# Optimization experiments

Measured on AMD Instinct MI355X. Metric: run time of the kernel, lower is better.

Reference implementation:

```python
import jax, jax.numpy as jnp
import numpy as np

# ---- config (matches init_kwargs) ----
GROUP_NUM = 2048
K_NEIGHBORS = 32
OUT_DIM = 192
SIGMA, BASELINE, SCALING, EPS = 0.26, 0.1, 10.0, 1e-6
ALPHA, BETA = 1000.0, 100.0
ADAPTIVE_RATIO = 0.5
IN_DIM = 3
ADAPTIVE_DIM = int(OUT_DIM * ADAPTIVE_RATIO)          # 96
FOURIER_DIM = OUT_DIM - ADAPTIVE_DIM                  # 96
FEAT_DIM_F = FOURIER_DIM // (IN_DIM * 2)              # 16
FEAT_DIM_A = int(np.ceil(ADAPTIVE_DIM / IN_DIM))      # 32
FEAT_NUM_A = FEAT_DIM_A * IN_DIM                      # 96
OUT_IDX = np.linspace(0, FEAT_NUM_A - 1, ADAPTIVE_DIM).astype(np.int64)


def setup_inputs() -> dict:
    key = jax.random.key(0)
    k1, k2, k3, k4 = jax.random.split(key, 4)
    xyz = jax.random.normal(k1, (4, 8192, 3), dtype=jnp.float32)
    x = jax.random.normal(k2, (4, 8192, 96), dtype=jnp.float32)
    bn_gamma = jax.random.uniform(k3, (192,), dtype=jnp.float32)
    bn_beta = jax.random.normal(k4, (192,), dtype=jnp.float32)
    return {"xyz": xyz, "x": x, "bn_gamma": bn_gamma, "bn_beta": bn_beta}


def _fps(xyz, m):
    """Farthest point sampling. xyz: [B,N,3] -> idx [B,m] (int32). Seed = index 0."""
    def single(pts):
        n = pts.shape[0]
        def step(carry, _):
            dists, last = carry
            d = jnp.sum((pts - pts[last]) ** 2, axis=-1)
            dists = jnp.minimum(dists, d)
            nxt = jnp.argmax(dists).astype(jnp.int32)
            return (dists, nxt), nxt
        init = (jnp.full((n,), 1e10, pts.dtype), jnp.array(0, jnp.int32))
        _, idxs = jax.lax.scan(step, init, None, length=m - 1)
        return jnp.concatenate([jnp.zeros((1,), jnp.int32), idxs])
    return jax.vmap(single)(xyz)


def _square_distance(src, dst):
    # src: [B,S,3], dst: [B,N,3] -> [B,S,N]
    d = -2.0 * jnp.einsum('bsc,bnc->bsn', src, dst)
    d += jnp.sum(src ** 2, -1)[:, :, None]
    d += jnp.sum(dst ** 2, -1)[:, None, :]
    return d


def _gather_knn(points, idx):
    # points: [B,N,C], idx: [B,G,K] -> [B,G,K,C]
    return jax.vmap(lambda p, i: p[i])(points, idx)


def _forward(xyz, x, bn_gamma, bn_beta):
    B, N, _ = xyz.shape
    G, K = GROUP_NUM, K_NEIGHBORS

    # ---- Grouper_seg ----
    fps_idx = _fps(xyz, G)                                   # [B,G]
    lc_xyz = jnp.take_along_axis(xyz, fps_idx[..., None], 1)  # [B,G,3]
    lc_x = jnp.take_along_axis(x, fps_idx[..., None], 1)      # [B,G,C]
    sqr = _square_distance(lc_xyz, xyz)                       # [B,G,N]
    knn_idx = jax.lax.top_k(-sqr, K)[1]                       # [B,G,K] smallest-k
    knn_xyz = _gather_knn(xyz, knn_idx)                       # [B,G,K,3]
    knn_x = _gather_knn(x, knn_idx)                           # [B,G,K,C]

    # ---- Aggregation_seg: local normalization ----
    mean_x = lc_x[:, :, None, :]
    std_x = jnp.std(knn_x - mean_x, ddof=1)
    mean_xyz = lc_xyz[:, :, None, :]
    std_xyz = jnp.std(knn_xyz - mean_xyz, ddof=1)
    knn_x = (knn_x - mean_x) / (std_x + 1e-5)
    knn_xyz_n = (knn_xyz - mean_xyz) / (std_xyz + 1e-5)       # [B,G,K,3]
    C = knn_x.shape[-1]
    knn_x = jnp.concatenate(
        [knn_x, jnp.broadcast_to(lc_x[:, :, None, :], (B, G, K, C))], axis=-1)  # [B,G,K,2C]
    knn_xyz_cf = jnp.transpose(knn_xyz_n, (0, 3, 1, 2))       # [B,3,G,K]
    knn_x_cf = jnp.transpose(knn_x, (0, 3, 1, 2))             # [B,OUT_DIM,G,K]

    # ---- PosE_Geo: fourier part ----
    feat_range = jnp.arange(FEAT_DIM_F, dtype=knn_xyz_cf.dtype)
    dim_embed = ALPHA ** (feat_range / FEAT_DIM_F)            # [F]
    div = BETA * knn_xyz_cf[..., None] / dim_embed            # [B,3,G,K,F]
    fourier = jnp.stack([jnp.sin(div), jnp.cos(div)], axis=-1)  # [B,3,G,K,F,2]
    fourier = fourier.reshape(B, IN_DIM, G, K, 2 * FEAT_DIM_F)
    fourier = jnp.transpose(fourier, (0, 1, 4, 2, 3)).reshape(B, FOURIER_DIM, G, K)

    # ---- AdaptiveEmbedding (parameterless, data-driven) ----
    x4 = knn_xyz_n                                            # [B,G,K,3]
    gstd = jnp.mean(jnp.std(x4.reshape(B, -1, IN_DIM), axis=1, ddof=1))
    sig = SIGMA * (1.0 + gstd) + EPS
    blend = jax.nn.sigmoid((gstd - BASELINE) * SCALING)
    feat_val = jnp.linspace(-1.0, 1.0, FEAT_DIM_A + 2)[1:-1]  # [Fa]
    z = (x4[..., None] - feat_val) / sig                      # [B,G,K,3,Fa]
    comb = blend * jnp.exp(-0.5 * z * z) + (1.0 - blend) * jnp.cos(z)
    ae = comb.reshape(B, G, K, FEAT_NUM_A)[..., OUT_IDX]      # [B,G,K,ADAPTIVE_DIM]
    ae_cf = jnp.transpose(ae, (0, 3, 1, 2))                   # [B,ADAPTIVE_DIM,G,K]

    pe = jnp.concatenate([fourier, ae_cf], axis=1)            # [B,OUT_DIM,G,K]
    knn_x_w = (knn_x_cf + pe) * pe

    # ---- Pooling_seg: max+mean pool, BatchNorm1d (train stats) + GELU ----
    lc = jnp.max(knn_x_w, -1) + jnp.mean(knn_x_w, -1)         # [B,OUT_DIM,G]
    mu = jnp.mean(lc, axis=(0, 2), keepdims=True)
    var = jnp.var(lc, axis=(0, 2), keepdims=True)
    y = (lc - mu) / jnp.sqrt(var + 1e-5)
    y = y * bn_gamma[None, :, None] + bn_beta[None, :, None]
    return jax.nn.gelu(y, approximate=False)


def reference(xyz, x, bn_gamma, bn_beta):
    return _forward(xyz, x, bn_gamma, bn_beta)
```

## Files before the change

### kernel.cpp

```cpp
#include <hip/hip_runtime.h>
#include <cstdint>
#include <math.h>

#define NPTS 8192
#define NB 4
#define NG 2048
#define NK 32
#define CIN 96
#define COUT 192

typedef unsigned long long ull;

__global__ __launch_bounds__(256) void setup_kernel(const float* __restrict__ xyz,
                                                    float* __restrict__ xs, float* __restrict__ ys,
                                                    float* __restrict__ zs, float* __restrict__ d2){
  int i = blockIdx.x*256 + threadIdx.x;
  if (i >= NB*NPTS) return;
  float x = xyz[3*i+0], y = xyz[3*i+1], z = xyz[3*i+2];
  xs[i]=x; ys[i]=y; zs[i]=z;
  d2[i] = __fadd_rn(__fadd_rn(__fmul_rn(x,x),__fmul_rn(y,y)),__fmul_rn(z,z));
}

template<int CTRL>
__device__ __forceinline__ ull dppmax64(ull v){
  unsigned lo=(unsigned)v, hi=(unsigned)(v>>32);
  unsigned olo=(unsigned)__builtin_amdgcn_update_dpp((int)lo,(int)lo,CTRL,0xf,0xf,false);
  unsigned ohi=(unsigned)__builtin_amdgcn_update_dpp((int)hi,(int)hi,CTRL,0xf,0xf,false);
  ull o=((ull)ohi<<32)|(ull)olo;
  return (o>v)?o:v;
}
__device__ __forceinline__ ull wavemax64(ull v){
  v=dppmax64<0x111>(v); v=dppmax64<0x112>(v); v=dppmax64<0x114>(v);
  v=dppmax64<0x118>(v); v=dppmax64<0x142>(v); v=dppmax64<0x143>(v);
  return v;
}

__global__ __launch_bounds__(512,2) void fps_kernel(const float* __restrict__ xyz, int* __restrict__ fps_idx){
#pragma clang fp contract(off)
  extern __shared__ char smem[];
  float4* ctab = (float4*)smem;
  ull*    keys = (ull*)(smem + 131072);
  int*    hist = (int*)(smem + 131072 + 128);
  float*  bbs  = (float*)(smem + 131072 + 128 + 2048);
  float*  bbc  = (float*)(smem + 131072 + 128 + 2048 + 192);
  const int b = blockIdx.x, t = threadIdx.x;
  const int w = t>>6, lane = t&63;
  const float* base = xyz + (size_t)b*NPTS*3;

  float ox[16], oy[16], oz[16];
#pragma unroll
  for (int j=0;j<16;++j){
    int p = t + 512*j;
    ox[j]=base[3*p+0]; oy[j]=base[3*p+1]; oz[j]=base[3*p+2];
  }
  float mnx=ox[0],mxx=ox[0],mny=oy[0],mxy=oy[0],mnz=oz[0],mxz=oz[0];
#pragma unroll
  for (int j=1;j<16;++j){
    mnx=fminf(mnx,ox[j]); mxx=fmaxf(mxx,ox[j]);
    mny=fminf(mny,oy[j]); mxy=fmaxf(mxy,oy[j]);
    mnz=fminf(mnz,oz[j]); mxz=fmaxf(mxz,oz[j]);
  }
#pragma unroll
  for (int off=32; off>0; off>>=1){
    mnx=fminf(mnx,__shfl_xor(mnx,off)); mxx=fmaxf(mxx,__shfl_xor(mxx,off));
    mny=fminf(mny,__shfl_xor(mny,off)); mxy=fmaxf(mxy,__shfl_xor(mxy,off));
    mnz=fminf(mnz,__shfl_xor(mnz,off)); mxz=fmaxf(mxz,__shfl_xor(mxz,off));
  }
  hist[t] = 0;
  if (lane==0){
    bbs[w*6+0]=mnx; bbs[w*6+1]=mxx; bbs[w*6+2]=mny;
    bbs[w*6+3]=mxy; bbs[w*6+4]=mnz; bbs[w*6+5]=mxz;
  }
  if (t==0) fps_idx[b*NG] = 0;
  __syncthreads();
  float gx0=1e30f,gx1=-1e30f,gy0=1e30f,gy1=-1e30f,gz0=1e30f,gz1=-1e30f;
  for (int q=0;q<8;++q){
    gx0=fminf(gx0,bbs[q*6+0]); gx1=fmaxf(gx1,bbs[q*6+1]);
    gy0=fminf(gy0,bbs[q*6+2]); gy1=fmaxf(gy1,bbs[q*6+3]);
    gz0=fminf(gz0,bbs[q*6+4]); gz1=fmaxf(gz1,bbs[q*6+5]);
  }
  const float sxv = 8.0f/fmaxf(gx1-gx0,1e-20f);
  const float syv = 8.0f/fmaxf(gy1-gy0,1e-20f);
  const float szv = 8.0f/fmaxf(gz1-gz0,1e-20f);
  int cell[16];
#pragma unroll
  for (int j=0;j<16;++j){
    int cx = min(7,(int)((ox[j]-gx0)*sxv));
    int cy = min(7,(int)((oy[j]-gy0)*syv));
    int cz = min(7,(int)((oz[j]-gz0)*szv));
    int m = (cx&1) | ((cy&1)<<1) | ((cz&1)<<2)
          | ((cx&2)<<2) | ((cy&2)<<3) | ((cz&2)<<4)
          | ((cx&4)<<4) | ((cy&4)<<5) | ((cz&4)<<6);
    cell[j]=m;
    atomicAdd(&hist[m],1);
  }
  __syncthreads();
  if (t==0){
    int run=0;
    for (int c=0;c<512;++c){ int h=hist[c]; hist[c]=run; run+=h; }
  }
  __syncthreads();
#pragma unroll
  for (int j=0;j<16;++j){
    int pos = atomicAdd(&hist[cell[j]],1);
    ctab[pos] = make_float4(ox[j],oy[j],oz[j], __int_as_float(t+512*j));
  }
  __syncthreads();
  float px[16],py[16],pz[16],D[16]; unsigned lowb[16];
#pragma unroll
  for (int j=0;j<16;++j){
    int pos = (w<<10) + (j<<6) + lane;
    float4 c4 = ctab[pos];
    px[j]=c4.x; py[j]=c4.y; pz[j]=c4.z;
    unsigned orig = (unsigned)__float_as_int(c4.w);
    lowb[j] = ((8191u-orig)<<13) | (unsigned)pos;
    D[j] = 1e10f;
  }
#pragma unroll
  for (int j=0;j<16;++j){
    float a0=px[j],a1=px[j],b0=py[j],b1=py[j],c0=pz[j],c1=pz[j];
#pragma unroll
    for (int off=32; off>0; off>>=1){
      a0=fminf(a0,__shfl_xor(a0,off)); a1=fmaxf(a1,__shfl_xor(a1,off));
      b0=fminf(b0,__shfl_xor(b0,off)); b1=fmaxf(b1,__shfl_xor(b1,off));
      c0=fminf(c0,__shfl_xor(c0,off)); c1=fmaxf(c1,__shfl_xor(c1,off));
    }
    if (lane==0){
      float* o = bbc + (w*16+j)*6;
      o[0]=a0; o[1]=a1; o[2]=b0; o[3]=b1; o[4]=c0; o[5]=c1;
    }
  }
  __syncthreads();
  float cb0=0,cb1=0,cb2=0,cb3=0,cb4=0,cb5=0;
  if (lane<16){
    const float* o = bbc + (w*16+lane)*6;
    cb0=o[0]; cb1=o[1]; cb2=o[2]; cb3=o[3]; cb4=o[4]; cb5=o[5];
  }

  float lx=base[0], ly=base[1], lz=base[2];
  ull ckey = (((ull)__float_as_uint(1e10f))<<32);
  for (int it=0; it<NG-1; ++it){
    float Mthr = __int_as_float((unsigned)(ckey>>32)) * 1.0001f;
    float qx=fminf(fmaxf(lx,cb0),cb1);
    float qy=fminf(fmaxf(ly,cb2),cb3);
    float qz=fminf(fmaxf(lz,cb4),cb5);
    float ddx=qx-lx, ddy=qy-ly, ddz=qz-lz;
    float LB=(ddx*ddx+ddy*ddy)+ddz*ddz;
    ull bal = __ballot(LB <= Mthr);
    unsigned mask = __builtin_amdgcn_readfirstlane((unsigned)bal) & 0xFFFFu;
    ull* kslot = &keys[(it&1)*8 + w];
    if (mask){
#pragma unroll
      for (int j=0;j<16;++j){
        if (mask & (1u<<j)){
          float dx=px[j]-lx, dy=py[j]-ly, dz=pz[j]-lz;
          float d=(dx*dx+dy*dy)+dz*dz;
          D[j]=fminf(D[j],d);
        }
      }
      ull P = (((ull)__float_as_uint(D[0]))<<32) | (ull)lowb[0];
#pragma unroll
      for (int j=1;j<16;++j){
        ull c = (((ull)__float_as_uint(D[j]))<<32) | (ull)lowb[j];
        if (c > P) P = c;
      }
      P = wavemax64(P);
      if (lane==63) *kslot = P;
      unsigned khi = (unsigned)__builtin_amdgcn_readlane((int)(P>>32),63);
      unsigned klo = (unsigned)__builtin_amdgcn_readlane((int)P,63);
      ckey = (((ull)khi)<<32)|(ull)klo;
    } else {
      if (lane==63) *kslot = ckey;
    }
    __syncthreads();
    const ull* kk = keys + (it&1)*8;
    ull k = kk[0];
#pragma unroll
    for (int q=1;q<8;++q){ ull o=kk[q]; if (o>k) k=o; }
    unsigned lw = (unsigned)k;
    float4 c4 = ctab[lw & 0x1FFFu];
    lx=c4.x; ly=c4.y; lz=c4.z;
    if (t==0) fps_idx[b*NG + it + 1] = (int)(8191u - ((lw>>13)&0x1FFFu));
  }
}

__device__ __forceinline__ bool lexlt(float ad, int ai, float bd, int bi){
  return (ad < bd) || ((ad == bd) && (ai < bi));
}
__device__ __forceinline__ void sort_desc(float& d, int& i, int lane){
#pragma unroll
  for (int k=2;k<=64;k<<=1){
#pragma unroll
    for (int j=k>>1;j>0;j>>=1){
      float od = __shfl_xor(d, j);
      int   oi = __shfl_xor(i, j);
      bool dirUp = (lane & k) != 0;
      bool lower = (lane & j) == 0;
      bool less  = lexlt(d,i,od,oi);
      bool keep  = (less == (lower == dirUp));
      if (!keep){ d=od; i=oi; }
    }
  }
}
__device__ __forceinline__ void merge_asc(float& d, int& i, int lane){
#pragma unroll
  for (int j=32;j>0;j>>=1){
    float od = __shfl_xor(d, j);
    int   oi = __shfl_xor(i, j);
    bool lower = (lane & j) == 0;
    bool less  = lexlt(d,i,od,oi);
    bool keep  = (less == lower);
    if (!keep){ d=od; i=oi; }
  }
}

__global__ __launch_bounds__(256) void knn_kernel(const float* __restrict__ xs, const float* __restrict__ ys,
                                                  const float* __restrict__ zs, const float* __restrict__ d2,
                                                  const int* __restrict__ fps_idx, int* __restrict__ knn_out){
  __shared__ float tx[256], ty[256], tz[256], td[256];
  const int tid = threadIdx.x;
  const int wid = tid>>6, lane = tid&63;
  const int pid = blockIdx.x*4 + wid;
  const int b = pid >> 11;
  const float* bx = xs + b*NPTS;
  const float* by = ys + b*NPTS;
  const float* bz = zs + b*NPTS;
  const float* bD = d2 + b*NPTS;
  const int fi = fps_idx[pid];
  const float ax = bx[fi], ay = by[fi], az = bz[fi];
  const float src2 = __fadd_rn(__fadd_rn(__fmul_rn(ax,ax),__fmul_rn(ay,ay)),__fmul_rn(az,az));
  float Ad = INFINITY; int Ai = 0x7fffffff;
  float tau_d = INFINITY; int tau_i = 0x7fffffff;
  for (int s=0; s<NPTS/256; ++s){
    __syncthreads();
    int gidx = s*256 + tid;
    tx[tid]=bx[gidx]; ty[tid]=by[gidx]; tz[tid]=bz[gidx]; td[tid]=bD[gidx];
    __syncthreads();
    float m0,m1,m2,m3; int i0,i1,i2,i3;
#define LOADJ(mj, ij, J) { int li = (J)*64 + lane; \
    float dot = __fadd_rn(__fadd_rn(__fmul_rn(ax,tx[li]),__fmul_rn(ay,ty[li])),__fmul_rn(az,tz[li])); \
    mj = __fadd_rn(__fadd_rn(__fmul_rn(-2.0f,dot), src2), td[li]); ij = s*256 + li; }
    LOADJ(m0,i0,0) LOADJ(m1,i1,1) LOADJ(m2,i2,2) LOADJ(m3,i3,3)
#undef LOADJ
    while (true){
      bool any = lexlt(m0,i0,tau_d,tau_i) || lexlt(m1,i1,tau_d,tau_i) ||
                 lexlt(m2,i2,tau_d,tau_i) || lexlt(m3,i3,tau_d,tau_i);
      if (__ballot(any) == 0ull) break;
      float cd = m0; int ci = i0; int sel = 0;
      if (lexlt(m1,i1,cd,ci)){ cd=m1; ci=i1; sel=1; }
      if (lexlt(m2,i2,cd,ci)){ cd=m2; ci=i2; sel=2; }
      if (lexlt(m3,i3,cd,ci)){ cd=m3; ci=i3; sel=3; }
      if      (sel==0) m0=INFINITY;
      else if (sel==1) m1=INFINITY;
      else if (sel==2) m2=INFINITY;
      else             m3=INFINITY;
      sort_desc(cd, ci, lane);
      if (lexlt(cd,ci,Ad,Ai)){ Ad=cd; Ai=ci; }
      merge_asc(Ad, Ai, lane);
      tau_d = __shfl(Ad, 31);
      tau_i = __shfl(Ai, 31);
    }
  }
  if (lane < NK) knn_out[pid*NK + lane] = Ai;
}

__global__ __launch_bounds__(256) void stats_kernel(const float* __restrict__ x, const float* __restrict__ xyz,
                                                    const int* __restrict__ fps_idx, const int* __restrict__ knn,
                                                    double* __restrict__ partials){
  const int tid=threadIdx.x, wid=tid>>6, lane=tid&63;
  const int pid = blockIdx.x*4 + wid;
  const int b = pid>>11;
  const int fi = fps_idx[pid];
  const float* xb = x + (size_t)b*NPTS*CIN;
  const float* zb = xyz + (size_t)b*NPTS*3;
  const float lc0 = xb[fi*CIN + lane];
  float lc1 = 0.f; if (lane<32) lc1 = xb[fi*CIN + 64 + lane];
  float czv = 0.f; if (lane<3)  czv = zb[fi*3 + lane];
  double s1=0.0, s2=0.0, a1=0.0, a2=0.0;
  for (int k=0;k<NK;++k){
    int idx = knn[pid*NK + k];
    float d0 = __fsub_rn(xb[idx*CIN + lane], lc0);
    s1 += (double)d0; s2 += (double)d0*(double)d0;
    if (lane<32){
      float d1 = __fsub_rn(xb[idx*CIN + 64 + lane], lc1);
      s1 += (double)d1; s2 += (double)d1*(double)d1;
    }
    if (lane<3){
      float w = __fsub_rn(zb[idx*3 + lane], czv);
      a1 += (double)w; a2 += (double)w*(double)w;
    }
  }
#pragma unroll
  for (int off=32; off>0; off>>=1){ s1 += __shfl_xor(s1,off); s2 += __shfl_xor(s2,off); }
  __shared__ double shx[4][2];
  __shared__ double shz[4][3][2];
  if (lane==0){ shx[wid][0]=s1; shx[wid][1]=s2; }
  if (lane<3){ shz[wid][lane][0]=a1; shz[wid][lane][1]=a2; }
  __syncthreads();
  if (tid==0){
    double u0=0,u1=0;
    for (int w=0;w<4;++w){ u0+=shx[w][0]; u1+=shx[w][1]; }
    double* outp = partials + (size_t)blockIdx.x*8;
    outp[0]=u0; outp[1]=u1;
    for (int axq=0; axq<3; ++axq){
      double v0=0,v1=0;
      for (int w=0;w<4;++w){ v0+=shz[w][axq][0]; v1+=shz[w][axq][1]; }
      outp[2+2*axq]=v0; outp[3+2*axq]=v1;
    }
  }
}

__global__ void finalize_kernel(const double* __restrict__ partials, float* __restrict__ scal){
  const int lane = threadIdx.x;
  double s1=0,s2=0;
  double z0a=0,z0b=0,z1a=0,z1b=0,z2a=0,z2b=0;
  for (int i=0;i<32;++i){
    const double* p = partials + (size_t)(lane*32+i)*8;
    s1+=p[0]; s2+=p[1];
    z0a+=p[2]; z0b+=p[3]; z1a+=p[4]; z1b+=p[5]; z2a+=p[6]; z2b+=p[7];
  }
#pragma unroll
  for (int off=32; off>0; off>>=1){ s1+=__shfl_xor(s1,off); s2+=__shfl_xor(s2,off); }
#pragma unroll
  for (int off=8; off>0; off>>=1){
    z0a+=__shfl_xor(z0a,off); z0b+=__shfl_xor(z0b,off);
    z1a+=__shfl_xor(z1a,off); z1b+=__shfl_xor(z1b,off);
    z2a+=__shfl_xor(z2a,off); z2b+=__shfl_xor(z2b,off);
  }
  __shared__ double zb[4][3][2];
  if ((lane&15)==0){
    int b = lane>>4;
    zb[b][0][0]=z0a; zb[b][0][1]=z0b;
    zb[b][1][0]=z1a; zb[b][1][1]=z1b;
    zb[b][2][0]=z2a; zb[b][2][1]=z2b;
  }
  __syncthreads();
  if (lane==0){
    double nx = (double)NB*NG*NK*CIN;
    double varx = (s2 - s1*s1/nx)/(nx-1.0);
    float stdx = (float)sqrt(varx);
    double t1=0,t2=0;
    for (int b=0;b<4;++b) for (int a=0;a<3;++a){ t1+=zb[b][a][0]; t2+=zb[b][a][1]; }
    double nz = (double)NB*NG*NK*3;
    double varz = (t2 - t1*t1/nz)/(nz-1.0);
    float stdz = (float)sqrt(varz);
    float sdiv = stdz + 1e-5f;
    double n2 = (double)NG*NK;
    double acc=0.0;
    for (int b=0;b<4;++b) for (int a=0;a<3;++a){
      double v = (zb[b][a][1] - zb[b][a][0]*zb[b][a][0]/n2)/(n2-1.0);
      acc += sqrt(v);
    }
    float gstd = (float)(acc/12.0) / sdiv;
    float sig = 0.26f*(1.0f+gstd) + 1e-6f;
    float blend = 1.0f/(1.0f + expf(-(gstd-0.1f)*10.0f));
    scal[0] = 1.0f/(stdx + 1e-5f);
    scal[1] = 1.0f/sdiv;
    scal[2] = 1.0f/sig;
    scal[3] = blend;
  }
}

__global__ __launch_bounds__(256) void main_kernel(const float* __restrict__ x, const float* __restrict__ xyz,
                                                   const int* __restrict__ fps_idx, const int* __restrict__ knn,
                                                   const float* __restrict__ scal, float* __restrict__ lc_out){
  const int tid=threadIdx.x, wid=tid>>6, lane=tid&63;
  const int pid = blockIdx.x*4 + wid;
  const int b = pid>>11, g = pid&2047;
  const float inv_x = scal[0], inv_z = scal[1], inv_sig = scal[2], blend = scal[3];
  const float omb = 1.0f - blend;
  const int fi = fps_idx[pid];
  const float* xb = x + (size_t)b*NPTS*CIN;
  const float* zb = xyz + (size_t)b*NPTS*3;
  const float cx = zb[fi*3+0], cy = zb[fi*3+1], cz = zb[fi*3+2];
  const float lcx0 = xb[fi*CIN + lane];
  const float lcx1 = (lane<32) ? xb[fi*CIN + 64 + lane] : xb[fi*CIN + lane - 32];
  const float lcx2 = xb[fi*CIN + 32 + lane];
  const int dim0 = lane>>5;
  const int rr0 = lane&31;
  const bool cos0 = rr0 & 1;
  const float bs0 = 100.0f / powf(1000.0f, (float)(rr0>>1) * (1.0f/16.0f));
  const bool cos1 = lane & 1;
  const float bs1 = 100.0f / powf(1000.0f, (float)((lane&31)>>1) * (1.0f/16.0f));
  const float fv1 = (float)(-1.0 + 2.0*(double)(lane-32+1)/33.0);
  const int dim2 = (32+lane)>>5;
  const int j2 = (32+lane)&31;
  const float fv2 = (float)(-1.0 + 2.0*(double)(j2+1)/33.0);

  float mx0=-INFINITY, mx1=-INFINITY, mx2=-INFINITY;
  float sm0=0.f, sm1=0.f, sm2=0.f;
  for (int k=0;k<NK;++k){
    const int idx = knn[pid*NK + k];
    const float p0 = zb[idx*3+0], p1 = zb[idx*3+1], p2v = zb[idx*3+2];
    const float xn0 = (p0-cx)*inv_z, xn1 = (p1-cy)*inv_z, xn2 = (p2v-cz)*inv_z;
    const float xk0 = xb[idx*CIN + lane];
    float xk1 = 0.f; if (lane<32) xk1 = xb[idx*CIN + 64 + lane];
    {
      float v = dim0 ? xn1 : xn0;
      float a = v * bs0;
      float pe = cos0 ? __cosf(a) : __sinf(a);
      float f = (xk0 - lcx0) * inv_x;
      float w = (f + pe) * pe;
      mx0 = fmaxf(mx0, w); sm0 += w;
    }
    {
      float pe, f;
      if (lane < 32){
        float a = xn2 * bs1;
        pe = cos1 ? __cosf(a) : __sinf(a);
        f = (xk1 - lcx1) * inv_x;
      } else {
        float zq = (xn0 - fv1) * inv_sig;
        pe = blend * __expf(-0.5f*zq*zq) + omb * __cosf(zq);
        f = lcx1;
      }
      float w = (f + pe) * pe;
      mx1 = fmaxf(mx1, w); sm1 += w;
    }
    {
      float v = (dim2==1) ? xn1 : xn2;
      float zq = (v - fv2) * inv_sig;
      float pe = blend * __expf(-0.5f*zq*zq) + omb * __cosf(zq);
      float w = (lcx2 + pe) * pe;
      mx2 = fmaxf(mx2, w); sm2 += w;
    }
  }
  const size_t obase = ((size_t)b*COUT)*NG + g;
  lc_out[obase + (size_t)lane*NG]       = mx0 + sm0*(1.0f/32.0f);
  lc_out[obase + (size_t)(64+lane)*NG]  = mx1 + sm1*(1.0f/32.0f);
  lc_out[obase + (size_t)(128+lane)*NG] = mx2 + sm2*(1.0f/32.0f);
}

__global__ __launch_bounds__(256) void bn_stats_kernel(const float* __restrict__ lc, float* __restrict__ bn){
  const int c = blockIdx.x, t = threadIdx.x, lane=t&63, wid=t>>6;
  double s1=0.0, s2=0.0;
  for (int i=t; i<NB*NG; i+=256){
    int b=i>>11, g=i&2047;
    float v = lc[((size_t)(b*COUT)+c)*NG + g];
    s1 += (double)v; s2 += (double)v*(double)v;
  }
#pragma unroll
  for (int off=32; off>0; off>>=1){ s1+=__shfl_xor(s1,off); s2+=__shfl_xor(s2,off); }
  __shared__ double sh1[4], sh2[4];
  if (lane==0){ sh1[wid]=s1; sh2[wid]=s2; }
  __syncthreads();
  if (t==0){
    double a=sh1[0]+sh1[1]+sh1[2]+sh1[3], q=sh2[0]+sh2[1]+sh2[2]+sh2[3];
    double n=(double)(NB*NG);
    double mu=a/n, var=q/n - mu*mu;
    bn[c]=(float)mu;
    bn[COUT+c]=(float)(1.0/sqrt(var + 1e-5));
  }
}

__global__ __launch_bounds__(256) void final_kernel(const float* __restrict__ bn, const float* __restrict__ gamma,
                                                    const float* __restrict__ beta, float* __restrict__ out){
  int i = blockIdx.x*256 + threadIdx.x;
  int c = (i >> 11) % COUT;
  float v = out[i];
  float y = (v - bn[c]) * bn[COUT + c];
  y = y*gamma[c] + beta[c];
  out[i] = y * 0.5f * (1.0f + erff(y * 0.70710678118654752f));
}

extern "C" void kernel_launch(void* const* d_in, const int* in_sizes, int n_in,
                              void* d_out, int out_size, void* d_ws, size_t ws_size,
                              hipStream_t stream){
  const float* xyz   = (const float*)d_in[0];
  const float* x     = (const float*)d_in[1];
  const float* gamma = (const float*)d_in[2];
  const float* beta  = (const float*)d_in[3];
  float* out = (float*)d_out;
  char* ws = (char*)d_ws;
  int*    fps  = (int*)   (ws + 0);
  int*    knn  = (int*)   (ws + 32768);
  float*  xs   = (float*) (ws + 1081344);
  float*  ys   = (float*) (ws + 1212416);
  float*  zs   = (float*) (ws + 1343488);
  float*  d2   = (float*) (ws + 1474560);
  double* parts= (double*)(ws + 1605632);
  float*  scal = (float*) (ws + 1736704);
  float*  bn   = (float*) (ws + 1736768);

  const int fps_lds = 131072 + 128 + 2048 + 192 + 3072;
  (void)hipFuncSetAttribute(reinterpret_cast<const void*>(fps_kernel),
                            hipFuncAttributeMaxDynamicSharedMemorySize, fps_lds);

  setup_kernel   <<<dim3((NB*NPTS+255)/256), dim3(256), 0, stream>>>(xyz, xs, ys, zs, d2);
  fps_kernel     <<<dim3(NB),                dim3(512), fps_lds, stream>>>(xyz, fps);
  knn_kernel     <<<dim3(NB*NG/4),           dim3(256), 0, stream>>>(xs, ys, zs, d2, fps, knn);
  stats_kernel   <<<dim3(NB*NG/4),           dim3(256), 0, stream>>>(x, xyz, fps, knn, parts);
  finalize_kernel<<<dim3(1),                 dim3(64),  0, stream>>>(parts, scal);
  main_kernel    <<<dim3(NB*NG/4),           dim3(256), 0, stream>>>(x, xyz, fps, knn, scal, out);
  bn_stats_kernel<<<dim3(COUT),              dim3(256), 0, stream>>>(out, bn);
  final_kernel   <<<dim3((NB*COUT*NG)/256),  dim3(256), 0, stream>>>(bn, gamma, beta, out);
}
```

Measured before the change: 2.550 ms.

## Rework FPS to per-chunk keys in LDS with dynamic work distribution

```diff
diff --git a/kernel.cpp b/kernel.cpp
--- a/kernel.cpp
+++ b/kernel.cpp
@@ -21,6 +21,8 @@
   d2[i] = __fadd_rn(__fadd_rn(__fmul_rn(x,x),__fmul_rn(y,y)),__fmul_rn(z,z));
 }
 
+__device__ __forceinline__ ull umax64(ull a, ull b){ return (a>b)?a:b; }
+
 template<int CTRL>
 __device__ __forceinline__ ull dppmax64(ull v){
   unsigned lo=(unsigned)v, hi=(unsigned)(v>>32);
@@ -35,14 +37,29 @@
   return v;
 }
 
+#define OFF_X    0
+#define OFF_Y    32768
+#define OFF_Z    65536
+#define OFF_D    98304
+#define OFF_ORG  131072
+#define OFF_K    147456
+#define OFF_BBC  149504
+#define OFF_HIST 153600
+#define OFF_BBS  155648
+#define FPS_LDS  155840
+
 __global__ __launch_bounds__(512,2) void fps_kernel(const float* __restrict__ xyz, int* __restrict__ fps_idx){
 #pragma clang fp contract(off)
   extern __shared__ char smem[];
-  float4* ctab = (float4*)smem;
-  ull*    keys = (ull*)(smem + 131072);
-  int*    hist = (int*)(smem + 131072 + 128);
-  float*  bbs  = (float*)(smem + 131072 + 128 + 2048);
-  float*  bbc  = (float*)(smem + 131072 + 128 + 2048 + 192);
+  float* X   = (float*)(smem + OFF_X);
+  float* Y   = (float*)(smem + OFF_Y);
+  float* Z   = (float*)(smem + OFF_Z);
+  float* Dar = (float*)(smem + OFF_D);
+  unsigned short* ORG = (unsigned short*)(smem + OFF_ORG);
+  ull*   Karr = (ull*)(smem + OFF_K);
+  float* bbc  = (float*)(smem + OFF_BBC);
+  int*   hist = (int*)(smem + OFF_HIST);
+  float* bbs  = (float*)(smem + OFF_BBS);
   const int b = blockIdx.x, t = threadIdx.x;
   const int w = t>>6, lane = t&63;
   const float* base = xyz + (size_t)b*NPTS*3;
@@ -67,6 +84,7 @@
     mnz=fminf(mnz,__shfl_xor(mnz,off)); mxz=fmaxf(mxz,__shfl_xor(mxz,off));
   }
   hist[t] = 0;
+  if (t < 128) Karr[128 + t] = ((ull)__float_as_uint(1e10f))<<32;
   if (lane==0){
     bbs[w*6+0]=mnx; bbs[w*6+1]=mxx; bbs[w*6+2]=mny;
     bbs[w*6+3]=mxy; bbs[w*6+4]=mnz; bbs[w*6+5]=mxz;
@@ -103,22 +121,14 @@
 #pragma unroll
   for (int j=0;j<16;++j){
     int pos = atomicAdd(&hist[cell[j]],1);
-    ctab[pos] = make_float4(ox[j],oy[j],oz[j], __int_as_float(t+512*j));
-  }
-  __syncthreads();
-  float px[16],py[16],pz[16],D[16]; unsigned lowb[16];
-#pragma unroll
+    X[pos]=ox[j]; Y[pos]=oy[j]; Z[pos]=oz[j];
+    ORG[pos]=(unsigned short)(t+512*j);
+    Dar[pos]=1e10f;
+  }
+  __syncthreads();
   for (int j=0;j<16;++j){
-    int pos = (w<<10) + (j<<6) + lane;
-    float4 c4 = ctab[pos];
-    px[j]=c4.x; py[j]=c4.y; pz[j]=c4.z;
-    unsigned orig = (unsigned)__float_as_int(c4.w);
-    lowb[j] = ((8191u-orig)<<13) | (unsigned)pos;
-    D[j] = 1e10f;
-  }
-#pragma unroll
-  for (int j=0;j<16;++j){
-    float a0=px[j],a1=px[j],b0=py[j],b1=py[j],c0=pz[j],c1=pz[j];
+    int c = (w<<4)+j, pos=(c<<6)+lane;
+    float a0=X[pos],a1=a0, b0=Y[pos],b1=b0, c0=Z[pos],c1=c0;
 #pragma unroll
     for (int off=32; off>0; off>>=1){
       a0=fminf(a0,__shfl_xor(a0,off)); a1=fmaxf(a1,__shfl_xor(a1,off));
@@ -126,61 +136,84 @@
       c0=fminf(c0,__shfl_xor(c0,off)); c1=fmaxf(c1,__shfl_xor(c1,off));
     }
     if (lane==0){
-      float* o = bbc + (w*16+j)*6;
-      o[0]=a0; o[1]=a1; o[2]=b0; o[3]=b1; o[4]=c0; o[5]=c1;
-    }
-  }
-  __syncthreads();
-  float cb0=0,cb1=0,cb2=0,cb3=0,cb4=0,cb5=0;
-  if (lane<16){
-    const float* o = bbc + (w*16+lane)*6;
-    cb0=o[0]; cb1=o[1]; cb2=o[2]; cb3=o[3]; cb4=o[4]; cb5=o[5];
-  }
+      float* o = bbc + c*8;
+      o[0]=a0; o[1]=a1; o[2]=b0; o[3]=b1; o[4]=c0; o[5]=c1; o[6]=0.f; o[7]=0.f;
+    }
+  }
+  __syncthreads();
+  float A0,A1,A2,A3,A4,A5, B0,B1,B2,B3,B4,B5;
+  { const float* o = bbc + lane*8;
+    A0=o[0];A1=o[1];A2=o[2];A3=o[3];A4=o[4];A5=o[5];
+    const float* p = bbc + (64+lane)*8;
+    B0=p[0];B1=p[1];B2=p[2];B3=p[3];B4=p[4];B5=p[5]; }
 
   float lx=base[0], ly=base[1], lz=base[2];
-  ull ckey = (((ull)__float_as_uint(1e10f))<<32);
   for (int it=0; it<NG-1; ++it){
-    float Mthr = __int_as_float((unsigned)(ckey>>32)) * 1.0001f;
-    float qx=fminf(fmaxf(lx,cb0),cb1);
-    float qy=fminf(fmaxf(ly,cb2),cb3);
-    float qz=fminf(fmaxf(lz,cb4),cb5);
-    float ddx=qx-lx, ddy=qy-ly, ddz=qz-lz;
-    float LB=(ddx*ddx+ddy*ddy)+ddz*ddz;
-    ull bal = __ballot(LB <= Mthr);
-    unsigned mask = __builtin_amdgcn_readfirstlane((unsigned)bal) & 0xFFFFu;
-    ull* kslot = &keys[(it&1)*8 + w];
-    if (mask){
-#pragma unroll
-      for (int j=0;j<16;++j){
-        if (mask & (1u<<j)){
-          float dx=px[j]-lx, dy=py[j]-ly, dz=pz[j]-lz;
-          float d=(dx*dx+dy*dy)+dz*dz;
-          D[j]=fminf(D[j],d);
-        }
+    ull* Knew = Karr + (it&1)*128;
+    const ull* Kold = Karr + ((it+1)&1)*128;
+    ull kA = Kold[lane], kB = Kold[64+lane];
+    float thrA = __int_as_float((int)(kA>>32)) * 1.0001f;
+    float thrB = __int_as_float((int)(kB>>32)) * 1.0001f;
+    float qx,qy,qz,ddx,ddy,ddz,LA,LBv;
+    qx=fminf(fmaxf(lx,A0),A1); qy=fminf(fmaxf(ly,A2),A3); qz=fminf(fmaxf(lz,A4),A5);
+    ddx=qx-lx; ddy=qy-ly; ddz=qz-lz; LA=(ddx*ddx+ddy*ddy)+ddz*ddz;
+    qx=fminf(fmaxf(lx,B0),B1); qy=fminf(fmaxf(ly,B2),B3); qz=fminf(fmaxf(lz,B4),B5);
+    ddx=qx-lx; ddy=qy-ly; ddz=qz-lz; LBv=(ddx*ddx+ddy*ddy)+ddz*ddz;
+    ull mA = __ballot(LA <= thrA);
+    ull mB = __ballot(LBv <= thrB);
+    if (lane < 16){
+      int c = (w<<4) + lane;
+      ull msel = (w<4)? mA : mB;
+      if (!((msel >> (c&63)) & 1ull)) Knew[c] = Kold[c];
+    }
+    int r = 0;
+    ull m0 = mA;
+    while (m0){
+      int c = __ffsll(m0) - 1;
+      m0 &= (m0 - 1);
+      if ((r & 7) == w){
+        int pos = (c<<6)|lane;
+        float x=X[pos], y=Y[pos], z=Z[pos], Do=Dar[pos];
+        float dx=x-lx, dy=y-ly, dz=z-lz;
+        float d=(dx*dx+dy*dy)+dz*dz;
+        float Dn=fminf(Do,d);
+        Dar[pos]=Dn;
+        unsigned orig=ORG[pos];
+        unsigned lowb=((8191u-orig)<<13)|(unsigned)pos;
+        ull key=(((ull)__float_as_uint(Dn))<<32)|(ull)lowb;
+        key=wavemax64(key);
+        if (lane==63) Knew[c]=key;
       }
-      ull P = (((ull)__float_as_uint(D[0]))<<32) | (ull)lowb[0];
-#pragma unroll
-      for (int j=1;j<16;++j){
-        ull c = (((ull)__float_as_uint(D[j]))<<32) | (ull)lowb[j];
-        if (c > P) P = c;
+      ++r;
+    }
+    ull m1 = mB;
+    while (m1){
+      int c = 64 + __ffsll(m1) - 1;
+      m1 &= (m1 - 1);
+      if ((r & 7) == w){
+        int pos = (c<<6)|lane;
+        float x=X[pos], y=Y[pos], z=Z[pos], Do=Dar[pos];
+        float dx=x-lx, dy=y-ly, dz=z-lz;
+        float d=(dx*dx+dy*dy)+dz*dz;
+        float Dn=fminf(Do,d);
+        Dar[pos]=Dn;
+        unsigned orig=ORG[pos];
+        unsigned lowb=((8191u-orig)<<13)|(unsigned)pos;
+        ull key=(((ull)__float_as_uint(Dn))<<32)|(ull)lowb;
+        key=wavemax64(key);
+        if (lane==63) Knew[c]=key;
       }
-      P = wavemax64(P);
-      if (lane==63) *kslot = P;
-      unsigned khi = (unsigned)__builtin_amdgcn_readlane((int)(P>>32),63);
-      unsigned klo = (unsigned)__builtin_amdgcn_readlane((int)P,63);
-      ckey = (((ull)khi)<<32)|(ull)klo;
-    } else {
-      if (lane==63) *kslot = ckey;
+      ++r;
     }
     __syncthreads();
-    const ull* kk = keys + (it&1)*8;
-    ull k = kk[0];
-#pragma unroll
-    for (int q=1;q<8;++q){ ull o=kk[q]; if (o>k) k=o; }
-    unsigned lw = (unsigned)k;
-    float4 c4 = ctab[lw & 0x1FFFu];
-    lx=c4.x; ly=c4.y; lz=c4.z;
-    if (t==0) fps_idx[b*NG + it + 1] = (int)(8191u - ((lw>>13)&0x1FFFu));
+    ull a = Knew[lane], b2 = Knew[64+lane];
+    ull k = wavemax64(umax64(a,b2));
+    unsigned khi = (unsigned)__builtin_amdgcn_readlane((int)(k>>32),63);
+    unsigned klo = (unsigned)__builtin_amdgcn_readlane((int)k,63);
+    (void)khi;
+    unsigned pos = klo & 0x1FFFu;
+    lx = X[pos]; ly = Y[pos]; lz = Z[pos];
+    if (t==0) fps_idx[b*NG + it + 1] = (int)(8191u - ((klo>>13)&0x1FFFu));
   }
 }
 
@@ -482,12 +515,11 @@
   float*  scal = (float*) (ws + 1736704);
   float*  bn   = (float*) (ws + 1736768);
 
-  const int fps_lds = 131072 + 128 + 2048 + 192 + 3072;
   (void)hipFuncSetAttribute(reinterpret_cast<const void*>(fps_kernel),
-                            hipFuncAttributeMaxDynamicSharedMemorySize, fps_lds);
+                            hipFuncAttributeMaxDynamicSharedMemorySize, FPS_LDS);
 
   setup_kernel   <<<dim3((NB*NPTS+255)/256), dim3(256), 0, stream>>>(xyz, xs, ys, zs, d2);
-  fps_kernel     <<<dim3(NB),                dim3(512), fps_lds, stream>>>(xyz, fps);
+  fps_kernel     <<<dim3(NB),                dim3(512), FPS_LDS, stream>>>(xyz, fps);
   knn_kernel     <<<dim3(NB*NG/4),           dim3(256), 0, stream>>>(xs, ys, zs, d2, fps, knn);
   stats_kernel   <<<dim3(NB*NG/4),           dim3(256), 0, stream>>>(x, xyz, fps, knn, parts);
   finalize_kernel<<<dim3(1),                 dim3(64),  0, stream>>>(parts, scal);
```

New measurement: 3.701 ms. +45.1%, slower.
